# Kernel tuning notes

Measured on AMD Instinct MI355X. Metric: run time of the kernel, lower is better.

The kernel has to match this reference:

```python
import jax, jax.numpy as jnp
import numpy as np

N, E, F, HID, HEADS, L, OUT = 25000, 400000, 128, 128, 2, 3, 10
C = HID // HEADS
EPS = 1e-5

def _ln(x, g, b):
    m = jnp.mean(x, -1, keepdims=True)
    v = jnp.mean((x - m) ** 2, -1, keepdims=True)
    return (x - m) / jnp.sqrt(v + EPS) * g + b

def _lrelu(x, s=0.01):
    return jnp.where(x >= 0, x, s * x)

def setup_inputs():
    key = jax.random.key(0)
    ks = iter(jax.random.split(key, 80))
    def nrm(shape, fan_in):
        return jax.random.normal(next(ks), shape, dtype=jnp.float32) / np.float32(np.sqrt(fan_in))
    return {
        "x": jax.random.normal(next(ks), (N, F), dtype=jnp.float32),
        "edge_index": jax.random.randint(next(ks), (2, E), 0, N, dtype=jnp.int32),
        "edge_attr": jax.random.uniform(next(ks), (E,), dtype=jnp.float32),
        "task_features": jax.random.normal(next(ks), (4,), dtype=jnp.float32),
        "emb_w": nrm((F, HID), F), "emb_b": jnp.zeros((HID,), jnp.float32),
        "emb_g": jnp.ones((HID,), jnp.float32), "emb_beta": jnp.zeros((HID,), jnp.float32),
        "gat_w": nrm((L, HID, HID), HID),
        "gat_as": nrm((L, HEADS, C), C), "gat_ad": nrm((L, HEADS, C), C),
        "gat_bias": jnp.zeros((L, HID), jnp.float32),
        "ec_w1": nrm((L, 2 * HID, HID), 2 * HID), "ec_b1": jnp.zeros((L, HID), jnp.float32),
        "ec_g1": jnp.ones((L, HID), jnp.float32), "ec_be1": jnp.zeros((L, HID), jnp.float32),
        "ec_w2": nrm((L, HID, HID), HID), "ec_b2": jnp.zeros((L, HID), jnp.float32),
        "ec_g2": jnp.ones((L, HID), jnp.float32), "ec_be2": jnp.zeros((L, HID), jnp.float32),
        "norm_g": jnp.ones((L, HID), jnp.float32), "norm_b": jnp.zeros((L, HID), jnp.float32),
        "task_w": nrm((4, HID), 4), "task_b": jnp.zeros((HID,), jnp.float32),
        "task_g": jnp.ones((HID,), jnp.float32), "task_beta": jnp.zeros((HID,), jnp.float32),
        "pa_w1": nrm((HID, HID // 2), HID), "pa_b1": jnp.zeros((HID // 2,), jnp.float32),
        "pa_w2": nrm((HID // 2, 1), HID // 2), "pa_b2": jnp.zeros((1,), jnp.float32),
        "v_w1": nrm((2 * HID, HID), 2 * HID), "v_b1": jnp.zeros((HID,), jnp.float32),
        "v_g": jnp.ones((HID,), jnp.float32), "v_be": jnp.zeros((HID,), jnp.float32),
        "v_w2": nrm((HID, 1), HID), "v_b2": jnp.zeros((1,), jnp.float32),
        "a_w1": nrm((2 * HID, HID), 2 * HID), "a_b1": jnp.zeros((HID,), jnp.float32),
        "a_g": jnp.ones((HID,), jnp.float32), "a_be": jnp.zeros((HID,), jnp.float32),
        "a_w2": nrm((HID, OUT), HID), "a_b2": jnp.zeros((OUT,), jnp.float32),
    }

def _forward(x, edge_attr, task_features, emb_w, emb_b, emb_g, emb_beta,
             gat_w, gat_as, gat_ad, gat_bias,
             ec_w1, ec_b1, ec_g1, ec_be1, ec_w2, ec_b2, ec_g2, ec_be2,
             norm_g, norm_b, task_w, task_b, task_g, task_beta,
             pa_w1, pa_b1, pa_w2, pa_b2,
             v_w1, v_b1, v_g, v_be, v_w2, v_b2,
             a_w1, a_b1, a_g, a_be, a_w2, a_b2, edge_index):
    src, dst = edge_index[0], edge_index[1]
    loop = jnp.arange(N, dtype=edge_index.dtype)
    src_sl = jnp.concatenate([src, loop])  # PyG GATConv adds self-loops
    dst_sl = jnp.concatenate([dst, loop])
    h = _lrelu(_ln(x @ emb_w + emb_b, emb_g, emb_beta))
    x0 = h
    for i in range(L):
        # --- GATConv (dropout inactive at eval) ---
        ht = (h @ gat_w[i]).reshape(N, HEADS, C)
        a_s = jnp.sum(ht * gat_as[i], -1)  # [N, HEADS]
        a_d = jnp.sum(ht * gat_ad[i], -1)
        e = _lrelu(a_s[src_sl] + a_d[dst_sl], 0.2)  # [E+N, HEADS]
        emax = jax.ops.segment_max(e, dst_sl, num_segments=N)
        ee = jnp.exp(e - emax[dst_sl])
        alpha = ee / jax.ops.segment_sum(ee, dst_sl, num_segments=N)[dst_sl]
        x1 = jax.ops.segment_sum(ht[src_sl] * alpha[:, :, None], dst_sl,
                                 num_segments=N).reshape(N, HID) + gat_bias[i]
        # --- EdgeConv: gather -> MLP -> weighted scatter-add ---
        ef = jnp.concatenate([h[src], h[dst]], axis=1)  # [E, 2*HID]
        ef = _lrelu(_ln(ef @ ec_w1[i] + ec_b1[i], ec_g1[i], ec_be1[i]), 0.2)
        ef = _lrelu(_ln(ef @ ec_w2[i] + ec_b2[i], ec_g2[i], ec_be2[i]), 0.2)
        ef = ef * edge_attr[:, None]
        x2 = jax.ops.segment_sum(ef, dst, num_segments=N)
        h = _lrelu(_ln(x1 + x2, norm_g[i], norm_b[i]))
        if i > 0:
            h = h + x0
            x0 = h
    # attention pooling over all nodes (batch=None path)
    w = jax.nn.softmax((_lrelu(h @ pa_w1 + pa_b1) @ pa_w2 + pa_b2)[:, 0])
    gf = jnp.sum(h * w[:, None], axis=0)  # [HID]
    te = _lrelu(_ln(task_features @ task_w + task_b, task_g, task_beta))
    cf = jnp.concatenate([gf, te], -1)  # [2*HID]
    value = _lrelu(_ln(cf @ v_w1 + v_b1, v_g, v_be)) @ v_w2 + v_b2
    adv = _lrelu(_ln(cf @ a_w1 + a_b1, a_g, a_be)) @ a_w2 + a_b2
    return value + (adv - jnp.mean(adv, -1, keepdims=True))

def reference(x, edge_index, edge_attr, task_features, emb_w, emb_b, emb_g, emb_beta, gat_w, gat_as, gat_ad, gat_bias, ec_w1, ec_b1, ec_g1, ec_be1, ec_w2, ec_b2, ec_g2, ec_be2, norm_g, norm_b, task_w, task_b, task_g, task_beta, pa_w1, pa_b1, pa_w2, pa_b2, v_w1, v_b1, v_g, v_be, v_w2, v_b2, a_w1, a_b1, a_g, a_be, a_w2, a_b2):
    return _forward(x, edge_attr, task_features, emb_w, emb_b, emb_g, emb_beta, gat_w, gat_as, gat_ad, gat_bias, ec_w1, ec_b1, ec_g1, ec_be1, ec_w2, ec_b2, ec_g2, ec_be2, norm_g, norm_b, task_w, task_b, task_g, task_beta, pa_w1, pa_b1, pa_w2, pa_b2, v_w1, v_b1, v_g, v_be, v_w2, v_b2, a_w1, a_b1, a_g, a_be, a_w2, a_b2, edge_index)
```

## Files before the change

### kernel.cpp

```cpp
#include <hip/hip_runtime.h>
#include <math.h>

#define NN 25000
#define EE 400000
#define LL 3
#define LNEPS 1e-5f
#define EB 64

typedef __attribute__((ext_vector_type(8))) short short8;
typedef __attribute__((ext_vector_type(16))) float f32x16;

__device__ __forceinline__ float lrelu(float x, float s) { return fmaxf(x, x * s); }

__device__ __forceinline__ unsigned int pack_bf2(float lo, float hi) {
    unsigned int ul = __float_as_uint(lo), uh = __float_as_uint(hi);
    ul = (ul + 0x7FFFu + ((ul >> 16) & 1u)) >> 16;
    uh = (uh + 0x7FFFu + ((uh >> 16) & 1u)) >> 16;
    return (uh << 16) | (ul & 0xFFFFu);
}
__device__ __forceinline__ float bf_lo(unsigned int u) { return __uint_as_float(u << 16); }
__device__ __forceinline__ float bf_hi(unsigned int u) { return __uint_as_float(u & 0xFFFF0000u); }

__device__ __forceinline__ void ln_stats128(float v, float* red, float& mean, float& inv) {
    float sm = v, sq = v * v;
#pragma unroll
    for (int m = 32; m >= 1; m >>= 1) { sm += __shfl_xor(sm, m); sq += __shfl_xor(sq, m); }
    __syncthreads();
    if ((threadIdx.x & 63) == 0) { red[(threadIdx.x >> 6) * 2] = sm; red[(threadIdx.x >> 6) * 2 + 1] = sq; }
    __syncthreads();
    sm = red[0] + red[2]; sq = red[1] + red[3];
    mean = sm * (1.f / 128.f);
    float var = sq * (1.f / 128.f) - mean * mean;
    inv = rsqrtf(var + LNEPS);
}

__global__ void k_hist(const int* __restrict__ dst, int* __restrict__ cnt, int ne)
{
    int i = blockIdx.x * 256 + threadIdx.x;
    if (i < ne) atomicAdd(&cnt[dst[i]], 1);
}

__global__ __launch_bounds__(1024) void k_scan(const int* __restrict__ cnt,
                                               int* __restrict__ starts, int n)
{
    __shared__ int tot[1024];
    int t = threadIdx.x;
    const int PER = (n + 1023) >> 10;
    int i0 = t * PER;
    int s = 0;
    for (int k = 0; k < PER; ++k) { int i = i0 + k; s += (i < n) ? cnt[i] : 0; }
    tot[t] = s;
    __syncthreads();
    for (int off = 1; off < 1024; off <<= 1) {
        int x = (t >= off) ? tot[t - off] : 0;
        __syncthreads();
        tot[t] += x;
        __syncthreads();
    }
    int run = (t > 0) ? tot[t - 1] : 0;
    for (int k = 0; k < PER; ++k) {
        int i = i0 + k;
        if (i < n) { starts[i] = run; run += cnt[i]; }
    }
    if (t == 1023) starts[n] = tot[1023];
}

__global__ void k_scatter(const int* __restrict__ src, const int* __restrict__ dst,
                          const float* __restrict__ ea, int* __restrict__ cursor,
                          int* __restrict__ s_src, int* __restrict__ s_dst,
                          float* __restrict__ s_ea, int ne)
{
    int i = blockIdx.x * 256 + threadIdx.x;
    if (i >= ne) return;
    int d = dst[i];
    int pos = atomicAdd(&cursor[d], 1);
    s_src[pos] = src[i];
    s_dst[pos] = d;
    s_ea[pos] = ea[i];
}

__global__ void k_prep(const float* __restrict__ gat_w, const float* __restrict__ ec_w1,
                       const float* __restrict__ ec_w2, const float* __restrict__ emb_w,
                       uint4* __restrict__ wf)
{
    int g = blockIdx.x * 256 + threadIdx.x;
    int m = g >> 11, f = g & 2047;
    const float* srcm;
    if (m < 3) srcm = gat_w + (size_t)m * 16384;
    else if (m < 9) { int t2 = m - 3; srcm = ec_w1 + (size_t)(t2 >> 1) * 32768 + (size_t)(t2 & 1) * 16384; }
    else if (m < 12) srcm = ec_w2 + (size_t)(m - 9) * 16384;
    else srcm = emb_w;
    int l = f & 63, ks = (f >> 6) & 7, nb = f >> 9;
    int k0 = ks * 16 + (l >> 5) * 8, col = nb * 32 + (l & 31);
    const float* wp = srcm + (size_t)k0 * 128 + col;
    uint4 r;
    r.x = pack_bf2(wp[0],   wp[128]);
    r.y = pack_bf2(wp[256], wp[384]);
    r.z = pack_bf2(wp[512], wp[640]);
    r.w = pack_bf2(wp[768], wp[896]);
    wf[g] = r;
}

__global__ __launch_bounds__(256) void k_emb(
    const float* __restrict__ in, const uint4* __restrict__ wfm,
    const float* __restrict__ bias, const float* __restrict__ g,
    const float* __restrict__ be, float* __restrict__ h,
    float* __restrict__ x0, int nrows)
{
    __shared__ __align__(16) unsigned int sA[64 * 64];
    __shared__ __align__(16) unsigned int sW[2048 * 4];
    float* sU = (float*)sW;
    const int tid = threadIdx.x;
    const int r0 = blockIdx.x * 64;
    {
        int row = tid >> 2, q = tid & 3;
        const float* srcp = in + (size_t)(r0 + row) * 128 + q * 32;
        bool ok = (r0 + row) < nrows;
#pragma unroll
        for (int i = 0; i < 8; ++i) {
            float4 v = ok ? *(const float4*)&srcp[i * 4] : make_float4(0.f, 0.f, 0.f, 0.f);
            int cu = (q * 16 + i * 2) ^ ((row & 15) << 2);
            *(uint2*)&sA[row * 64 + cu] = make_uint2(pack_bf2(v.x, v.y), pack_bf2(v.z, v.w));
        }
    }
    {
        uint4* sW4 = (uint4*)sW;
#pragma unroll
        for (int i = 0; i < 8; ++i) sW4[tid + 256 * i] = wfm[tid + 256 * i];
    }
    __syncthreads();
    const int w = tid >> 6, l = tid & 63;
    const int m0 = (w >> 1) * 32, nhalf = (w & 1);
    f32x16 acc0 = {}, acc1 = {};
#pragma unroll
    for (int ks = 0; ks < 8; ++ks) {
        int rw = m0 + (l & 31);
        int cu = (ks * 8 + (l >> 5) * 4) ^ ((rw & 15) << 2);
        short8 a = *(const short8*)&sA[rw * 64 + cu];
        short8 b0 = *(const short8*)&sW[((nhalf * 16 + ks) * 64 + l) * 4];
        short8 b1 = *(const short8*)&sW[(((nhalf * 2 + 1) * 8 + ks) * 64 + l) * 4];
        acc0 = __builtin_amdgcn_mfma_f32_32x32x16_bf16(a, b0, acc0, 0, 0, 0);
        acc1 = __builtin_amdgcn_mfma_f32_32x32x16_bf16(a, b1, acc1, 0, 0, 0);
    }
    __syncthreads();
    {
        int colbase = nhalf * 64 + (l & 31);
        float bb0 = bias[colbase], bb1 = bias[colbase + 32];
#pragma unroll
        for (int r = 0; r < 16; ++r) {
            int rw = m0 + (r & 3) + 8 * (r >> 2) + 4 * (l >> 5);
            sU[rw * 128 + colbase]      = acc0[r] + bb0;
            sU[rw * 128 + colbase + 32] = acc1[r] + bb1;
        }
    }
    __syncthreads();
    float2 gv = *(const float2*)&g[l * 2];
    float2 bv = *(const float2*)&be[l * 2];
    for (int it = 0; it < 16; ++it) {
        int rw = w * 16 + it;
        int grow = r0 + rw;
        if (grow >= nrows) break;
        float2 v = *(const float2*)&sU[rw * 128 + l * 2];
        float sm = v.x + v.y, sq = v.x * v.x + v.y * v.y;
#pragma unroll
        for (int m = 32; m >= 1; m >>= 1) { sm += __shfl_xor(sm, m); sq += __shfl_xor(sq, m); }
        float mean = sm * (1.f / 128.f);
        float var = sq * (1.f / 128.f) - mean * mean;
        float inv = rsqrtf(var + LNEPS);
        float o0 = lrelu((v.x - mean) * inv * gv.x + bv.x, 0.01f);
        float o1 = lrelu((v.y - mean) * inv * gv.y + bv.y, 0.01f);
        unsigned off = (unsigned)grow * 128u + (unsigned)(l * 2);
        *(float2*)&h[off]  = make_float2(o0, o1);
        *(float2*)&x0[off] = make_float2(o0, o1);
    }
}

__global__ __launch_bounds__(256) void k_gemm3(
    const float* __restrict__ in, const uint4* __restrict__ wf,
    int mht, int mA, int mB, const float* __restrict__ bA,
    unsigned* __restrict__ o0, unsigned* __restrict__ o1, unsigned* __restrict__ o2,
    int nrows)
{
    __shared__ __align__(16) unsigned int sA[64 * 64];
    __shared__ __align__(16) unsigned int sW[2048 * 4];
    const int tid = threadIdx.x;
    const int r0 = blockIdx.x * 64;
    {
        int row = tid >> 2, q = tid & 3;
        const float* srcp = in + (size_t)(r0 + row) * 128 + q * 32;
        bool ok = (r0 + row) < nrows;
#pragma unroll
        for (int i = 0; i < 8; ++i) {
            float4 v = ok ? *(const float4*)&srcp[i * 4] : make_float4(0.f, 0.f, 0.f, 0.f);
            unsigned int p0 = pack_bf2(v.x, v.y), p1 = pack_bf2(v.z, v.w);
            int cu = (q * 16 + i * 2) ^ ((row & 15) << 2);
            *(uint2*)&sA[row * 64 + cu] = make_uint2(p0, p1);
        }
    }
    __syncthreads();
    const int w = tid >> 6, l = tid & 63;
    const int m0 = (w >> 1) * 32, nhalf = (w & 1);
    short8 af[8];
#pragma unroll
    for (int ks = 0; ks < 8; ++ks) {
        int row = m0 + (l & 31);
        int cu = (ks * 8 + (l >> 5) * 4) ^ ((row & 15) << 2);
        af[ks] = *(const short8*)&sA[row * 64 + cu];
    }
    const int c = l & 31;
    const bool evenl = (c & 1) == 0;
    const unsigned uidx = (unsigned)(nhalf * 32 + (evenl ? (c >> 1) : (16 + (c >> 1))));
    auto do_mat = [&](int mat, unsigned* out, const float* bp) {
        __syncthreads();
        {
            const uint4* wsrc = wf + (size_t)mat * 2048;
            uint4* sW4 = (uint4*)sW;
#pragma unroll
            for (int i = 0; i < 8; ++i) sW4[tid + 256 * i] = wsrc[tid + 256 * i];
        }
        __syncthreads();
        f32x16 acc0 = {}, acc1 = {};
        const int nb0 = nhalf * 2;
#pragma unroll
        for (int ks = 0; ks < 8; ++ks) {
            short8 b0 = *(const short8*)&sW[((nb0 * 8 + ks) * 64 + l) * 4];
            short8 b1v = *(const short8*)&sW[(((nb0 + 1) * 8 + ks) * 64 + l) * 4];
            acc0 = __builtin_amdgcn_mfma_f32_32x32x16_bf16(af[ks], b0, acc0, 0, 0, 0);
            acc1 = __builtin_amdgcn_mfma_f32_32x32x16_bf16(af[ks], b1v, acc1, 0, 0, 0);
        }
        int colbase = nhalf * 64 + c;
        float badd0 = bp ? bp[colbase] : 0.f;
        float badd1 = bp ? bp[colbase + 32] : 0.f;
#pragma unroll
        for (int r = 0; r < 16; ++r) {
            float v0 = acc0[r] + badd0;
            float v1 = acc1[r] + badd1;
            float v0p = __shfl_xor(v0, 1);
            float v1p = __shfl_xor(v1, 1);
            int row = r0 + m0 + (r & 3) + 8 * (r >> 2) + 4 * (l >> 5);
            if (row < nrows) {
                unsigned val = evenl ? pack_bf2(v0, v0p) : pack_bf2(v1p, v1);
                out[(unsigned)row * 64u + uidx] = val;
            }
        }
    };
    do_mat(mht, o0, nullptr);
    do_mat(mA, o1, bA);
    do_mat(mB, o2, nullptr);
}

__global__ __launch_bounds__(512) void k_node_scores(
    const unsigned* __restrict__ htp, const unsigned* __restrict__ Apk,
    const unsigned* __restrict__ Bpk,
    const float* __restrict__ as_, const float* __restrict__ ad_,
    float* __restrict__ a_s, float* __restrict__ a_d,
    float* __restrict__ denom, float* __restrict__ selfe,
    float* __restrict__ rsA, float* __restrict__ rsB, int n)
{
    int wv = threadIdx.x >> 6, ln = threadIdx.x & 63;
    int node = blockIdx.x * 8 + wv;
    if (node >= n) return;
    unsigned off = (unsigned)node * 64u + (unsigned)ln;
    unsigned hv = htp[off], av = Apk[off], bv = Bpk[off];
    float h0 = bf_lo(hv), h1 = bf_hi(hv);
    float2 wsv = *(const float2*)&as_[ln * 2];
    float2 wdv = *(const float2*)&ad_[ln * 2];
    float ss = h0 * wsv.x + h1 * wsv.y;
    float sd = h0 * wdv.x + h1 * wdv.y;
    float sa = bf_lo(av) + bf_hi(av), sb = bf_lo(bv) + bf_hi(bv);
#pragma unroll
    for (int m = 16; m >= 1; m >>= 1) {
        ss += __shfl_xor(ss, m); sd += __shfl_xor(sd, m);
        sa += __shfl_xor(sa, m); sb += __shfl_xor(sb, m);
    }
    float sa2 = sa + __shfl_xor(sa, 32);
    float sb2 = sb + __shfl_xor(sb, 32);
    if ((ln & 31) == 0) {
        int hd = ln >> 5;
        a_s[node * 2 + hd] = ss;
        a_d[node * 2 + hd] = sd;
        float ev = expf(lrelu(ss + sd, 0.2f));
        denom[node * 2 + hd] = ev;
        selfe[node * 2 + hd] = ev;
        if (hd == 0) { rsA[node] = sa2; rsB[node] = sb2; }
    }
}

__global__ void k_edge_denom2(const int* __restrict__ s_src, const int* __restrict__ s_dst,
                              const float* __restrict__ a_s, const float* __restrict__ a_d,
                              float* __restrict__ denom, int ne)
{
    int base = (blockIdx.x * 256 + threadIdx.x) * 8;
    if (base >= ne) return;
    int curd = -1;
    float acc0 = 0.f, acc1 = 0.f;
    for (int k = 0; k < 8; ++k) {
        int e = base + k;
        if (e >= ne) break;
        int s = s_src[e], d = s_dst[e];
        float v0 = expf(lrelu(a_s[(unsigned)(s * 2)]     + a_d[(unsigned)(d * 2)],     0.2f));
        float v1 = expf(lrelu(a_s[(unsigned)(s * 2 + 1)] + a_d[(unsigned)(d * 2 + 1)], 0.2f));
        if (d != curd) {
            if (curd >= 0) { atomicAdd(&denom[curd * 2], acc0); atomicAdd(&denom[curd * 2 + 1], acc1); }
            curd = d; acc0 = v0; acc1 = v1;
        } else { acc0 += v0; acc1 += v1; }
    }
    if (curd >= 0) { atomicAdd(&denom[curd * 2], acc0); atomicAdd(&denom[curd * 2 + 1], acc1); }
}

__global__ void k_xsum_init(const unsigned* __restrict__ htp, const float* __restrict__ selfe,
                            const float* __restrict__ denom,
                            const float* __restrict__ gbias, float* __restrict__ xsum, int n)
{
    unsigned idx = blockIdx.x * blockDim.x + threadIdx.x;
    if (idx >= (unsigned)n * 64u) return;
    unsigned node = idx >> 6, u = idx & 63, hd = u >> 5;
    float alpha = selfe[node * 2 + hd] / denom[node * 2 + hd];
    unsigned hv = htp[idx];
    float2 o;
    o.x = gbias[u * 2]     + bf_lo(hv) * alpha;
    o.y = gbias[u * 2 + 1] + bf_hi(hv) * alpha;
    *(float2*)&xsum[node * 128u + u * 2u] = o;
}

__global__ __launch_bounds__(512) void k_edge_main(
    const unsigned* __restrict__ Apk, const unsigned* __restrict__ Bpk,
    const unsigned* __restrict__ htp,
    const int* __restrict__ s_src, const int* __restrict__ s_dst,
    const float* __restrict__ s_ea,
    const float* __restrict__ a_s, const float* __restrict__ a_d,
    const float* __restrict__ denom,
    const uint4* __restrict__ w2f,
    const float* __restrict__ rsA, const float* __restrict__ rsB,
    const float* __restrict__ g1, const float* __restrict__ be1,
    const float* __restrict__ b2, const float* __restrict__ g2, const float* __restrict__ be2,
    float* __restrict__ xsum, int ne)
{
    __shared__ __align__(16) unsigned int sWB[2048 * 4];
    __shared__ __align__(16) unsigned int sT32[EB * 64];
    __shared__ int   sS[EB], sD[EB];
    __shared__ float sEA[EB], sM[EB];
    __shared__ float sAl[EB * 2];
    __shared__ float sG1[128], sE1[128], sB2[128], sG2[128], sE2[128];
    float* sU = (float*)sWB;

    const int tid = threadIdx.x;
    {
        uint4* sWB4 = (uint4*)sWB;
#pragma unroll
        for (int i = 0; i < 4; ++i) { int f = tid + 512 * i; sWB4[f] = w2f[f]; }
    }
    if (tid < 128) {
        sG1[tid] = g1[tid]; sE1[tid] = be1[tid];
        sB2[tid] = b2[tid]; sG2[tid] = g2[tid]; sE2[tid] = be2[tid];
    }
    const int e0 = blockIdx.x * EB;
    const int nev = (ne - e0 < EB) ? (ne - e0) : EB;
    if (tid < EB) {
        if (tid < nev) {
            int s = s_src[e0 + tid], d = s_dst[e0 + tid];
            sS[tid] = s; sD[tid] = d; sEA[tid] = s_ea[e0 + tid];
            sM[tid] = (rsA[s] + rsB[d]) * (1.f / 128.f);
        } else { sS[tid] = 0; sD[tid] = -1; sEA[tid] = 0.f; sM[tid] = 0.f; }
    }
    if (tid < 2 * EB) {
        int le = tid >> 1, hd = tid & 1;
        float al = 0.f;
        if (le < nev) {
            int e = e0 + le;
            int s = s_src[e], d = s_dst[e];
            float ev = lrelu(a_s[(unsigned)(s * 2 + hd)] + a_d[(unsigned)(d * 2 + hd)], 0.2f);
            al = expf(ev) / denom[(unsigned)(d * 2 + hd)];
        }
        sAl[le * 2 + hd] = al;
    }
    __syncthreads();

    const int wv = tid >> 6, ln = tid & 63;
    {
        const float g1a = sG1[ln * 2], g1b = sG1[ln * 2 + 1];
        const float e1a = sE1[ln * 2], e1b = sE1[ln * 2 + 1];
        for (int j = 0; j < 8; ++j) {
            int e = wv * 8 + j;
            if (e < nev) {
                unsigned s = (unsigned)sS[e], d = (unsigned)sD[e];
                float mean = sM[e];
                unsigned av = Apk[s * 64u + ln];
                unsigned bv = Bpk[d * 64u + ln];
                float v0 = bf_lo(av) + bf_lo(bv) - mean;
                float v1 = bf_hi(av) + bf_hi(bv) - mean;
                float sq = v0 * v0 + v1 * v1;
#pragma unroll
                for (int m = 32; m >= 1; m >>= 1) sq += __shfl_xor(sq, m);
                float inv = rsqrtf(sq * (1.f / 128.f) + LNEPS);
                float t0 = lrelu(v0 * inv * g1a + e1a, 0.2f);
                float t1 = lrelu(v1 * inv * g1b + e1b, 0.2f);
                sT32[e * 64 + (ln ^ ((e & 15) << 2))] = pack_bf2(t0, t1);
            }
        }
    }
    __syncthreads();

    {
        const int w = wv, l = ln;
        const int m0 = (w >> 2) * 32, n0 = (w & 3) * 32;
        f32x16 acc = {};
#pragma unroll
        for (int ks = 0; ks < 8; ++ks) {
            int row = m0 + (l & 31);
            int colu = (ks * 8 + (l >> 5) * 4) ^ ((row & 15) << 2);
            short8 a = *(const short8*)&sT32[row * 64 + colu];
            short8 b = *(const short8*)&sWB[((((w & 3) * 8 + ks) * 64 + l)) * 4];
            acc = __builtin_amdgcn_mfma_f32_32x32x16_bf16(a, b, acc, 0, 0, 0);
        }
        __syncthreads();
        float b2c = sB2[n0 + (l & 31)];
#pragma unroll
        for (int r = 0; r < 16; ++r) {
            int row = m0 + (r & 3) + 8 * (r >> 2) + 4 * (l >> 5);
            sU[row * 128 + n0 + (l & 31)] = acc[r] + b2c;
        }
    }
    __syncthreads();

    {
        const unsigned ln2 = (unsigned)(ln * 2);
        const float g2a = sG2[ln * 2], g2b = sG2[ln * 2 + 1];
        const float e2a = sE2[ln * 2], e2b = sE2[ln * 2 + 1];
        int curd = -1;
        float acc0 = 0.f, acc1 = 0.f;
        for (int j = 0; j < 8; ++j) {
            int e = wv * 8 + j;
            if (e >= nev) break;
            unsigned s = (unsigned)sS[e];
            int d = sD[e];
            float2 uv = *(const float2*)&sU[e * 128 + ln * 2];
            float u0 = uv.x, u1 = uv.y;
            float sm = u0 + u1, sq = u0 * u0 + u1 * u1;
#pragma unroll
            for (int m = 32; m >= 1; m >>= 1) { sm += __shfl_xor(sm, m); sq += __shfl_xor(sq, m); }
            float mean = sm * (1.f / 128.f);
            float var = sq * (1.f / 128.f) - mean * mean;
            float inv = rsqrtf(var + LNEPS);
            float eav = sEA[e];
            float v0 = lrelu((u0 - mean) * inv * g2a + e2a, 0.2f) * eav;
            float v1 = lrelu((u1 - mean) * inv * g2b + e2b, 0.2f) * eav;
            float al = sAl[e * 2 + (ln >> 5)];
            unsigned hv = htp[s * 64u + ln];
            v0 += bf_lo(hv) * al;
            v1 += bf_hi(hv) * al;
            if (d != curd) {
                if (curd >= 0) {
                    atomicAdd(&xsum[(unsigned)curd * 128u + ln2], acc0);
                    atomicAdd(&xsum[(unsigned)curd * 128u + ln2 + 1], acc1);
                }
                curd = d; acc0 = v0; acc1 = v1;
            } else { acc0 += v0; acc1 += v1; }
        }
        if (curd >= 0) {
            atomicAdd(&xsum[(unsigned)curd * 128u + ln2], acc0);
            atomicAdd(&xsum[(unsigned)curd * 128u + ln2 + 1], acc1);
        }
    }
}

__global__ __launch_bounds__(512) void k_norm8(const float* __restrict__ xsum,
                                               const float* __restrict__ g,
                                               const float* __restrict__ b,
                                               float* __restrict__ x0,
                                               float* __restrict__ h, int n, int layer)
{
    int wv = threadIdx.x >> 6, ln = threadIdx.x & 63;
    int node = blockIdx.x * 8 + wv;
    if (node >= n) return;
    unsigned off = (unsigned)node * 128u + (unsigned)(ln * 2);
    float2 v = *(const float2*)&xsum[off];
    float sm = v.x + v.y, sq = v.x * v.x + v.y * v.y;
#pragma unroll
    for (int m = 32; m >= 1; m >>= 1) { sm += __shfl_xor(sm, m); sq += __shfl_xor(sq, m); }
    float mean = sm * (1.f / 128.f);
    float var = sq * (1.f / 128.f) - mean * mean;
    float inv = rsqrtf(var + LNEPS);
    float2 gv = *(const float2*)&g[ln * 2];
    float2 bv = *(const float2*)&b[ln * 2];
    float val0 = lrelu((v.x - mean) * inv * gv.x + bv.x, 0.01f);
    float val1 = lrelu((v.y - mean) * inv * gv.y + bv.y, 0.01f);
    if (layer > 0) {
        float2 x0v = *(const float2*)&x0[off];
        val0 += x0v.x; val1 += x0v.y;
        *(float2*)&x0[off] = make_float2(val0, val1);
    }
    *(float2*)&h[off] = make_float2(val0, val1);
}

__global__ __launch_bounds__(256) void k_pool_score(const float* __restrict__ h,
    const float* __restrict__ w1, const float* __restrict__ b1,
    const float* __restrict__ w2, const float* __restrict__ b2,
    float* __restrict__ score, int n)
{
    int wv = threadIdx.x >> 6, ln = threadIdx.x & 63;
    int node = blockIdx.x * 4 + wv;
    if (node >= n) return;
    float acc = b1[ln];
    const float* hr = h + (size_t)node * 128;
    for (int k = 0; k < 128; ++k) acc += hr[k] * w1[k * 64 + ln];
    acc = lrelu(acc, 0.01f) * w2[ln];
#pragma unroll
    for (int m = 32; m >= 1; m >>= 1) acc += __shfl_xor(acc, m);
    if (ln == 0) score[node] = acc + b2[0];
}

__global__ __launch_bounds__(256) void k_softmax_reduce(const float* __restrict__ score,
                                                        float* __restrict__ stats,
                                                        float* __restrict__ gf, int n)
{
    __shared__ float red[8];
    int t = threadIdx.x;
    float mx = -1e30f;
    for (int i = t; i < n; i += 256) mx = fmaxf(mx, score[i]);
#pragma unroll
    for (int m = 32; m >= 1; m >>= 1) mx = fmaxf(mx, __shfl_xor(mx, m));
    if ((t & 63) == 0) red[t >> 6] = mx;
    __syncthreads();
    mx = fmaxf(fmaxf(red[0], red[1]), fmaxf(red[2], red[3]));
    float s = 0.f;
    for (int i = t; i < n; i += 256) s += expf(score[i] - mx);
#pragma unroll
    for (int m = 32; m >= 1; m >>= 1) s += __shfl_xor(s, m);
    if ((t & 63) == 0) red[4 + (t >> 6)] = s;
    __syncthreads();
    s = red[4] + red[5] + red[6] + red[7];
    if (t == 0) { stats[0] = mx; stats[1] = s; }
    if (t < 128) gf[t] = 0.f;
}

__global__ __launch_bounds__(128) void k_gf(const float* __restrict__ h,
                                            const float* __restrict__ score,
                                            const float* __restrict__ stats,
                                            float* __restrict__ gf, int n)
{
    int c = threadIdx.x;
    float mx = stats[0], invZ = 1.f / stats[1];
    int per = (n + gridDim.x - 1) / gridDim.x;
    int n0 = blockIdx.x * per;
    int n1 = n0 + per; if (n1 > n) n1 = n;
    float acc = 0.f;
    for (int i = n0; i < n1; ++i)
        acc += expf(score[i] - mx) * invZ * h[(size_t)i * 128 + c];
    atomicAdd(&gf[c], acc);
}

__global__ __launch_bounds__(128) void k_head(
    const float* __restrict__ gf, const float* __restrict__ tf,
    const float* __restrict__ task_w, const float* __restrict__ task_b,
    const float* __restrict__ task_g, const float* __restrict__ task_be,
    const float* __restrict__ v_w1, const float* __restrict__ v_b1,
    const float* __restrict__ v_g, const float* __restrict__ v_be,
    const float* __restrict__ v_w2, const float* __restrict__ v_b2,
    const float* __restrict__ a_w1, const float* __restrict__ a_b1,
    const float* __restrict__ a_g, const float* __restrict__ a_be,
    const float* __restrict__ a_w2, const float* __restrict__ a_b2,
    float* __restrict__ out)
{
    __shared__ float cf[256], hbuf[128], red[4], sc[2], adv[10];
    int t = threadIdx.x;
    float mean, inv;
    float te = task_b[t];
#pragma unroll
    for (int k = 0; k < 4; ++k) te += tf[k] * task_w[k * 128 + t];
    ln_stats128(te, red, mean, inv);
    te = lrelu((te - mean) * inv * task_g[t] + task_be[t], 0.01f);
    cf[t] = gf[t]; cf[128 + t] = te;
    __syncthreads();
    float v = v_b1[t];
    for (int k = 0; k < 256; ++k) v += cf[k] * v_w1[k * 128 + t];
    ln_stats128(v, red, mean, inv);
    v = lrelu((v - mean) * inv * v_g[t] + v_be[t], 0.01f);
    float pv = v * v_w2[t];
#pragma unroll
    for (int m = 32; m >= 1; m >>= 1) pv += __shfl_xor(pv, m);
    __syncthreads();
    if ((t & 63) == 0) red[t >> 6] = pv;
    __syncthreads();
    if (t == 0) sc[0] = red[0] + red[1] + v_b2[0];
    float a = a_b1[t];
    for (int k = 0; k < 256; ++k) a += cf[k] * a_w1[k * 128 + t];
    ln_stats128(a, red, mean, inv);
    a = lrelu((a - mean) * inv * a_g[t] + a_be[t], 0.01f);
    hbuf[t] = a;
    __syncthreads();
    if (t < 10) {
        float s = a_b2[t];
        for (int c = 0; c < 128; ++c) s += hbuf[c] * a_w2[c * 10 + t];
        adv[t] = s;
    }
    __syncthreads();
    if (t == 0) {
        float m10 = 0.f;
        for (int o = 0; o < 10; ++o) m10 += adv[o];
        sc[1] = m10 * 0.1f;
    }
    __syncthreads();
    if (t < 10) out[t] = sc[0] + adv[t] - sc[1];
}

extern "C" void kernel_launch(void* const* d_in, const int* in_sizes, int n_in,
                              void* d_out, int out_size, void* d_ws, size_t ws_size,
                              hipStream_t stream)
{
    const float* x        = (const float*)d_in[0];
    const int*   ei       = (const int*)d_in[1];
    const float* ea       = (const float*)d_in[2];
    const float* tf       = (const float*)d_in[3];
    const float* emb_w    = (const float*)d_in[4];
    const float* emb_b    = (const float*)d_in[5];
    const float* emb_g    = (const float*)d_in[6];
    const float* emb_beta = (const float*)d_in[7];
    const float* gat_w    = (const float*)d_in[8];
    const float* gat_as   = (const float*)d_in[9];
    const float* gat_ad   = (const float*)d_in[10];
    const float* gat_bias = (const float*)d_in[11];
    const float* ec_w1    = (const float*)d_in[12];
    const float* ec_b1    = (const float*)d_in[13];
    const float* ec_g1    = (const float*)d_in[14];
    const float* ec_be1   = (const float*)d_in[15];
    const float* ec_w2    = (const float*)d_in[16];
    const float* ec_b2    = (const float*)d_in[17];
    const float* ec_g2    = (const float*)d_in[18];
    const float* ec_be2   = (const float*)d_in[19];
    const float* norm_g   = (const float*)d_in[20];
    const float* norm_b   = (const float*)d_in[21];
    const float* task_w   = (const float*)d_in[22];
    const float* task_b   = (const float*)d_in[23];
    const float* task_g   = (const float*)d_in[24];
    const float* task_be  = (const float*)d_in[25];
    const float* pa_w1    = (const float*)d_in[26];
    const float* pa_b1    = (const float*)d_in[27];
    const float* pa_w2    = (const float*)d_in[28];
    const float* pa_b2    = (const float*)d_in[29];
    const float* v_w1     = (const float*)d_in[30];
    const float* v_b1     = (const float*)d_in[31];
    const float* v_g      = (const float*)d_in[32];
    const float* v_be     = (const float*)d_in[33];
    const float* v_w2     = (const float*)d_in[34];
    const float* v_b2     = (const float*)d_in[35];
    const float* a_w1     = (const float*)d_in[36];
    const float* a_b1     = (const float*)d_in[37];
    const float* a_g      = (const float*)d_in[38];
    const float* a_be     = (const float*)d_in[39];
    const float* a_w2     = (const float*)d_in[40];
    const float* a_b2     = (const float*)d_in[41];

    const int n = in_sizes[0] / 128;
    const int e = in_sizes[2];
    const int* src = ei;
    const int* dst = ei + e;

    float* ws = (float*)d_ws;
    uint4* wf = (uint4*)ws;
    float* base = ws + 13 * 2048 * 4;
    const size_t NR = (size_t)n * 128;
    const size_t NP = (size_t)n * 64;
    float* h    = base;
    float* x0   = base + NR;
    float* xs   = base + 2 * NR;
    unsigned* htp = (unsigned*)(base + 3 * NR);
    unsigned* Apk = htp + NP;
    unsigned* Bpk = Apk + NP;
    float* a_s  = (float*)(Bpk + NP);
    float* a_d  = a_s + (size_t)n * 2;
    float* den  = a_d + (size_t)n * 2;
    float* selfe = den + (size_t)n * 2;
    float* rsA  = selfe + (size_t)n * 2;
    float* rsB  = rsA + n;
    float* score = rsB + n;
    float* stats = score + n;
    float* gf    = stats + 2;
    int*   cnt    = (int*)(gf + 128);
    int*   starts = cnt + n;
    int*   s_src  = starts + (n + 1);
    int*   s_dst  = s_src + e;
    float* s_ea   = (float*)(s_dst + e);

    const int ng64 = (n + 63) / 64;
    const int ng8 = (n + 7) / 8;

    hipMemsetAsync(cnt, 0, (size_t)n * sizeof(int), stream);
    k_hist<<<(e + 255) / 256, 256, 0, stream>>>(dst, cnt, e);
    k_scan<<<1, 1024, 0, stream>>>(cnt, starts, n);
    hipMemcpyAsync(cnt, starts, (size_t)n * sizeof(int), hipMemcpyDeviceToDevice, stream);
    k_scatter<<<(e + 255) / 256, 256, 0, stream>>>(src, dst, ea, cnt, s_src, s_dst, s_ea, e);
    k_prep<<<104, 256, 0, stream>>>(gat_w, ec_w1, ec_w2, emb_w, wf);

    k_emb<<<ng64, 256, 0, stream>>>(x, wf + (size_t)12 * 2048, emb_b, emb_g, emb_beta, h, x0, n);

    for (int i = 0; i < LL; ++i) {
        k_gemm3<<<ng64, 256, 0, stream>>>(h, wf, i, 3 + 2 * i, 4 + 2 * i,
                                          ec_b1 + i * 128, htp, Apk, Bpk, n);
        k_node_scores<<<ng8, 512, 0, stream>>>(htp, Apk, Bpk, gat_as + i * 128, gat_ad + i * 128,
                                               a_s, a_d, den, selfe, rsA, rsB, n);
        k_edge_denom2<<<((e + 7) / 8 + 255) / 256, 256, 0, stream>>>(s_src, s_dst, a_s, a_d, den, e);
        k_xsum_init<<<(n * 64 + 255) / 256, 256, 0, stream>>>(htp, selfe, den,
                                                              gat_bias + i * 128, xs, n);
        k_edge_main<<<(e + EB - 1) / EB, 512, 0, stream>>>(Apk, Bpk, htp, s_src, s_dst, s_ea,
                                                           a_s, a_d, den,
                                                           wf + (size_t)(9 + i) * 2048,
                                                           rsA, rsB,
                                                           ec_g1 + i * 128, ec_be1 + i * 128,
                                                           ec_b2 + i * 128, ec_g2 + i * 128, ec_be2 + i * 128,
                                                           xs, e);
        k_norm8<<<ng8, 512, 0, stream>>>(xs, norm_g + i * 128, norm_b + i * 128, x0, h, n, i);
    }

    k_pool_score<<<(n + 3) / 4, 256, 0, stream>>>(h, pa_w1, pa_b1, pa_w2, pa_b2, score, n);
    k_softmax_reduce<<<1, 256, 0, stream>>>(score, stats, gf, n);
    k_gf<<<200, 128, 0, stream>>>(h, score, stats, gf, n);
    k_head<<<1, 128, 0, stream>>>(gf, tf, task_w, task_b, task_g, task_be,
                                  v_w1, v_b1, v_g, v_be, v_w2, v_b2,
                                  a_w1, a_b1, a_g, a_be, a_w2, a_b2,
                                  (float*)d_out);
}
```

Baseline: 798.1 us.

## Fuse xsum init into norm, cache edge exps, compute LN mean via MFMA

```diff
diff --git a/kernel.cpp b/kernel.cpp
--- a/kernel.cpp
+++ b/kernel.cpp
@@ -81,24 +81,44 @@
 
 __global__ void k_prep(const float* __restrict__ gat_w, const float* __restrict__ ec_w1,
                        const float* __restrict__ ec_w2, const float* __restrict__ emb_w,
-                       uint4* __restrict__ wf)
-{
-    int g = blockIdx.x * 256 + threadIdx.x;
-    int m = g >> 11, f = g & 2047;
-    const float* srcm;
-    if (m < 3) srcm = gat_w + (size_t)m * 16384;
-    else if (m < 9) { int t2 = m - 3; srcm = ec_w1 + (size_t)(t2 >> 1) * 32768 + (size_t)(t2 & 1) * 16384; }
-    else if (m < 12) srcm = ec_w2 + (size_t)(m - 9) * 16384;
-    else srcm = emb_w;
-    int l = f & 63, ks = (f >> 6) & 7, nb = f >> 9;
-    int k0 = ks * 16 + (l >> 5) * 8, col = nb * 32 + (l & 31);
-    const float* wp = srcm + (size_t)k0 * 128 + col;
-    uint4 r;
-    r.x = pack_bf2(wp[0],   wp[128]);
-    r.y = pack_bf2(wp[256], wp[384]);
-    r.z = pack_bf2(wp[512], wp[640]);
-    r.w = pack_bf2(wp[768], wp[896]);
-    wf[g] = r;
+                       const float* __restrict__ ec_b2,
+                       uint4* __restrict__ wf, float* __restrict__ w2rs,
+                       float* __restrict__ b2s)
+{
+    int bid = blockIdx.x;
+    if (bid < 104) {
+        int g = bid * 256 + threadIdx.x;
+        int m = g >> 11, f = g & 2047;
+        const float* srcm;
+        if (m < 3) srcm = gat_w + (size_t)m * 16384;
+        else if (m < 9) { int t2 = m - 3; srcm = ec_w1 + (size_t)(t2 >> 1) * 32768 + (size_t)(t2 & 1) * 16384; }
+        else if (m < 12) srcm = ec_w2 + (size_t)(m - 9) * 16384;
+        else srcm = emb_w;
+        int l = f & 63, ks = (f >> 6) & 7, nb = f >> 9;
+        int k0 = ks * 16 + (l >> 5) * 8, col = nb * 32 + (l & 31);
+        const float* wp = srcm + (size_t)k0 * 128 + col;
+        uint4 r;
+        r.x = pack_bf2(wp[0],   wp[128]);
+        r.y = pack_bf2(wp[256], wp[384]);
+        r.z = pack_bf2(wp[512], wp[640]);
+        r.w = pack_bf2(wp[768], wp[896]);
+        wf[g] = r;
+    } else {
+        int gi = (bid - 104) * 256 + threadIdx.x;
+        if (gi < 384) {
+            int mt = gi >> 7, k = gi & 127;
+            const float* wp = ec_w2 + (size_t)mt * 16384 + (size_t)k * 128;
+            float s = 0.f;
+            for (int j = 0; j < 128; ++j) s += bf_lo(pack_bf2(wp[j], 0.f));
+            w2rs[mt * 128 + k] = s;
+        } else if (gi < 387) {
+            int mt = gi - 384;
+            const float* bp = ec_b2 + mt * 128;
+            float s = 0.f;
+            for (int j = 0; j < 128; ++j) s += bp[j];
+            b2s[mt] = s;
+        }
+    }
 }
 
 __global__ __launch_bounds__(256) void k_emb(
@@ -288,9 +308,13 @@
 
 __global__ void k_edge_denom2(const int* __restrict__ s_src, const int* __restrict__ s_dst,
                               const float* __restrict__ a_s, const float* __restrict__ a_d,
-                              float* __restrict__ denom, int ne)
-{
-    int base = (blockIdx.x * 256 + threadIdx.x) * 8;
+                              float* __restrict__ denom, float* __restrict__ expo,
+                              float4* __restrict__ xz, int nz4, int ne)
+{
+    int gtid = blockIdx.x * 256 + threadIdx.x;
+    for (int i = gtid; i < nz4; i += gridDim.x * 256)
+        xz[i] = make_float4(0.f, 0.f, 0.f, 0.f);
+    int base = gtid * 8;
     if (base >= ne) return;
     int curd = -1;
     float acc0 = 0.f, acc1 = 0.f;
@@ -300,27 +324,13 @@
         int s = s_src[e], d = s_dst[e];
         float v0 = expf(lrelu(a_s[(unsigned)(s * 2)]     + a_d[(unsigned)(d * 2)],     0.2f));
         float v1 = expf(lrelu(a_s[(unsigned)(s * 2 + 1)] + a_d[(unsigned)(d * 2 + 1)], 0.2f));
+        *(float2*)&expo[(unsigned)e * 2] = make_float2(v0, v1);
         if (d != curd) {
             if (curd >= 0) { atomicAdd(&denom[curd * 2], acc0); atomicAdd(&denom[curd * 2 + 1], acc1); }
             curd = d; acc0 = v0; acc1 = v1;
         } else { acc0 += v0; acc1 += v1; }
     }
     if (curd >= 0) { atomicAdd(&denom[curd * 2], acc0); atomicAdd(&denom[curd * 2 + 1], acc1); }
-}
-
-__global__ void k_xsum_init(const unsigned* __restrict__ htp, const float* __restrict__ selfe,
-                            const float* __restrict__ denom,
-                            const float* __restrict__ gbias, float* __restrict__ xsum, int n)
-{
-    unsigned idx = blockIdx.x * blockDim.x + threadIdx.x;
-    if (idx >= (unsigned)n * 64u) return;
-    unsigned node = idx >> 6, u = idx & 63, hd = u >> 5;
-    float alpha = selfe[node * 2 + hd] / denom[node * 2 + hd];
-    unsigned hv = htp[idx];
-    float2 o;
-    o.x = gbias[u * 2]     + bf_lo(hv) * alpha;
-    o.y = gbias[u * 2 + 1] + bf_hi(hv) * alpha;
-    *(float2*)&xsum[node * 128u + u * 2u] = o;
 }
 
 __global__ __launch_bounds__(512) void k_edge_main(
@@ -328,9 +338,9 @@
     const unsigned* __restrict__ htp,
     const int* __restrict__ s_src, const int* __restrict__ s_dst,
     const float* __restrict__ s_ea,
-    const float* __restrict__ a_s, const float* __restrict__ a_d,
-    const float* __restrict__ denom,
+    const float* __restrict__ expo, const float* __restrict__ denom,
     const uint4* __restrict__ w2f,
+    const float* __restrict__ w2rs, const float* __restrict__ b2sum,
     const float* __restrict__ rsA, const float* __restrict__ rsB,
     const float* __restrict__ g1, const float* __restrict__ be1,
     const float* __restrict__ b2, const float* __restrict__ g2, const float* __restrict__ be2,
@@ -341,6 +351,9 @@
     __shared__ int   sS[EB], sD[EB];
     __shared__ float sEA[EB], sM[EB];
     __shared__ float sAl[EB * 2];
+    __shared__ float sMean[EB];
+    __shared__ __align__(16) unsigned int sRS[64];
+    __shared__ float sB2S[1];
     __shared__ float sG1[128], sE1[128], sB2[128], sG2[128], sE2[128];
     float* sU = (float*)sWB;
 
@@ -354,6 +367,8 @@
         sG1[tid] = g1[tid]; sE1[tid] = be1[tid];
         sB2[tid] = b2[tid]; sG2[tid] = g2[tid]; sE2[tid] = be2[tid];
     }
+    if (tid < 64) sRS[tid] = pack_bf2(w2rs[tid * 2], w2rs[tid * 2 + 1]);
+    if (tid == 64) sB2S[0] = b2sum[0];
     const int e0 = blockIdx.x * EB;
     const int nev = (ne - e0 < EB) ? (ne - e0) : EB;
     if (tid < EB) {
@@ -368,9 +383,8 @@
         float al = 0.f;
         if (le < nev) {
             int e = e0 + le;
-            int s = s_src[e], d = s_dst[e];
-            float ev = lrelu(a_s[(unsigned)(s * 2 + hd)] + a_d[(unsigned)(d * 2 + hd)], 0.2f);
-            al = expf(ev) / denom[(unsigned)(d * 2 + hd)];
+            int d = s_dst[e];
+            al = expo[(unsigned)e * 2 + hd] / denom[(unsigned)(d * 2 + hd)];
         }
         sAl[le * 2 + hd] = al;
     }
@@ -404,7 +418,8 @@
     {
         const int w = wv, l = ln;
         const int m0 = (w >> 2) * 32, n0 = (w & 3) * 32;
-        f32x16 acc = {};
+        const bool dostat = (w & 3) == 0;
+        f32x16 acc = {}, accS = {};
 #pragma unroll
         for (int ks = 0; ks < 8; ++ks) {
             int row = m0 + (l & 31);
@@ -412,6 +427,18 @@
             short8 a = *(const short8*)&sT32[row * 64 + colu];
             short8 b = *(const short8*)&sWB[((((w & 3) * 8 + ks) * 64 + l)) * 4];
             acc = __builtin_amdgcn_mfma_f32_32x32x16_bf16(a, b, acc, 0, 0, 0);
+            if (dostat) {
+                short8 brs = *(const short8*)&sRS[ks * 8 + (l >> 5) * 4];
+                accS = __builtin_amdgcn_mfma_f32_32x32x16_bf16(a, brs, accS, 0, 0, 0);
+            }
+        }
+        if (dostat && (l & 31) == 0) {
+            float b2sv = sB2S[0];
+#pragma unroll
+            for (int r = 0; r < 16; ++r) {
+                int row = m0 + (r & 3) + 8 * (r >> 2) + 4 * (l >> 5);
+                sMean[row] = (accS[r] + b2sv) * (1.f / 128.f);
+            }
         }
         __syncthreads();
         float b2c = sB2[n0 + (l & 31)];
@@ -434,17 +461,16 @@
             if (e >= nev) break;
             unsigned s = (unsigned)sS[e];
             int d = sD[e];
+            float mean = sMean[e];
             float2 uv = *(const float2*)&sU[e * 128 + ln * 2];
-            float u0 = uv.x, u1 = uv.y;
-            float sm = u0 + u1, sq = u0 * u0 + u1 * u1;
-#pragma unroll
-            for (int m = 32; m >= 1; m >>= 1) { sm += __shfl_xor(sm, m); sq += __shfl_xor(sq, m); }
-            float mean = sm * (1.f / 128.f);
-            float var = sq * (1.f / 128.f) - mean * mean;
-            float inv = rsqrtf(var + LNEPS);
+            float v0c = uv.x - mean, v1c = uv.y - mean;
+            float sq = v0c * v0c + v1c * v1c;
+#pragma unroll
+            for (int m = 32; m >= 1; m >>= 1) sq += __shfl_xor(sq, m);
+            float inv = rsqrtf(sq * (1.f / 128.f) + LNEPS);
             float eav = sEA[e];
-            float v0 = lrelu((u0 - mean) * inv * g2a + e2a, 0.2f) * eav;
-            float v1 = lrelu((u1 - mean) * inv * g2b + e2b, 0.2f) * eav;
+            float v0 = lrelu(v0c * inv * g2a + e2a, 0.2f) * eav;
+            float v1 = lrelu(v1c * inv * g2b + e2b, 0.2f) * eav;
             float al = sAl[e * 2 + (ln >> 5)];
             unsigned hv = htp[s * 64u + ln];
             v0 += bf_lo(hv) * al;
@@ -465,6 +491,10 @@
 }
 
 __global__ __launch_bounds__(512) void k_norm8(const float* __restrict__ xsum,
+                                               const unsigned* __restrict__ htp,
+                                               const float* __restrict__ selfe,
+                                               const float* __restrict__ denom,
+                                               const float* __restrict__ gbias,
                                                const float* __restrict__ g,
                                                const float* __restrict__ b,
                                                float* __restrict__ x0,
@@ -474,7 +504,13 @@
     int node = blockIdx.x * 8 + wv;
     if (node >= n) return;
     unsigned off = (unsigned)node * 128u + (unsigned)(ln * 2);
+    int hd = ln >> 5;
+    float alpha = selfe[node * 2 + hd] / denom[node * 2 + hd];
+    unsigned hv = htp[(unsigned)node * 64u + (unsigned)ln];
+    float2 gb = *(const float2*)&gbias[ln * 2];
     float2 v = *(const float2*)&xsum[off];
+    v.x += gb.x + bf_lo(hv) * alpha;
+    v.y += gb.y + bf_hi(hv) * alpha;
     float sm = v.x + v.y, sq = v.x * v.x + v.y * v.y;
 #pragma unroll
     for (int m = 32; m >= 1; m >>= 1) { sm += __shfl_xor(sm, m); sq += __shfl_xor(sq, m); }
@@ -681,16 +717,20 @@
     int*   s_src  = starts + (n + 1);
     int*   s_dst  = s_src + e;
     float* s_ea   = (float*)(s_dst + e);
+    float* expo   = s_ea + e;
+    float* w2rs   = expo + (size_t)2 * e;
+    float* b2sum  = w2rs + 384;
 
     const int ng64 = (n + 63) / 64;
     const int ng8 = (n + 7) / 8;
+    const int ngd = ((e + 7) / 8 + 255) / 256;
 
     hipMemsetAsync(cnt, 0, (size_t)n * sizeof(int), stream);
     k_hist<<<(e + 255) / 256, 256, 0, stream>>>(dst, cnt, e);
     k_scan<<<1, 1024, 0, stream>>>(cnt, starts, n);
     hipMemcpyAsync(cnt, starts, (size_t)n * sizeof(int), hipMemcpyDeviceToDevice, stream);
     k_scatter<<<(e + 255) / 256, 256, 0, stream>>>(src, dst, ea, cnt, s_src, s_dst, s_ea, e);
-    k_prep<<<104, 256, 0, stream>>>(gat_w, ec_w1, ec_w2, emb_w, wf);
+    k_prep<<<106, 256, 0, stream>>>(gat_w, ec_w1, ec_w2, emb_w, ec_b2, wf, w2rs, b2sum);
 
     k_emb<<<ng64, 256, 0, stream>>>(x, wf + (size_t)12 * 2048, emb_b, emb_g, emb_beta, h, x0, n);
 
@@ -699,17 +739,18 @@
                                           ec_b1 + i * 128, htp, Apk, Bpk, n);
         k_node_scores<<<ng8, 512, 0, stream>>>(htp, Apk, Bpk, gat_as + i * 128, gat_ad + i * 128,
                                                a_s, a_d, den, selfe, rsA, rsB, n);
-        k_edge_denom2<<<((e + 7) / 8 + 255) / 256, 256, 0, stream>>>(s_src, s_dst, a_s, a_d, den, e);
-        k_xsum_init<<<(n * 64 + 255) / 256, 256, 0, stream>>>(htp, selfe, den,
-                                                              gat_bias + i * 128, xs, n);
+        k_edge_denom2<<<ngd, 256, 0, stream>>>(s_src, s_dst, a_s, a_d, den, expo,
+                                               (float4*)xs, n * 32, e);
         k_edge_main<<<(e + EB - 1) / EB, 512, 0, stream>>>(Apk, Bpk, htp, s_src, s_dst, s_ea,
-                                                           a_s, a_d, den,
+                                                           expo, den,
                                                            wf + (size_t)(9 + i) * 2048,
+                                                           w2rs + i * 128, b2sum + i,
                                                            rsA, rsB,
                                                            ec_g1 + i * 128, ec_be1 + i * 128,
                                                            ec_b2 + i * 128, ec_g2 + i * 128, ec_be2 + i * 128,
                                                            xs, e);
-        k_norm8<<<ng8, 512, 0, stream>>>(xs, norm_g + i * 128, norm_b + i * 128, x0, h, n, i);
+        k_norm8<<<ng8, 512, 0, stream>>>(xs, htp, selfe, den, gat_bias + i * 128,
+                                         norm_g + i * 128, norm_b + i * 128, x0, h, n, i);
     }
 
     k_pool_score<<<(n + 3) / 4, 256, 0, stream>>>(h, pa_w1, pa_b1, pa_w2, pa_b2, score, n);
```

New measurement: 904.0 us. 13.3% more time.

## Fold xsum init into norm kernel and cache edge exponentials

Applied to the files above, without the earlier changes.

```diff
diff --git a/kernel.cpp b/kernel.cpp
--- a/kernel.cpp
+++ b/kernel.cpp
@@ -288,9 +288,13 @@
 
 __global__ void k_edge_denom2(const int* __restrict__ s_src, const int* __restrict__ s_dst,
                               const float* __restrict__ a_s, const float* __restrict__ a_d,
-                              float* __restrict__ denom, int ne)
-{
-    int base = (blockIdx.x * 256 + threadIdx.x) * 8;
+                              float* __restrict__ denom, float* __restrict__ expo,
+                              float4* __restrict__ xz, int nz4, int ne)
+{
+    int gtid = blockIdx.x * 256 + threadIdx.x;
+    for (int i = gtid; i < nz4; i += gridDim.x * 256)
+        xz[i] = make_float4(0.f, 0.f, 0.f, 0.f);
+    int base = gtid * 8;
     if (base >= ne) return;
     int curd = -1;
     float acc0 = 0.f, acc1 = 0.f;
@@ -300,27 +304,13 @@
         int s = s_src[e], d = s_dst[e];
         float v0 = expf(lrelu(a_s[(unsigned)(s * 2)]     + a_d[(unsigned)(d * 2)],     0.2f));
         float v1 = expf(lrelu(a_s[(unsigned)(s * 2 + 1)] + a_d[(unsigned)(d * 2 + 1)], 0.2f));
+        *(float2*)&expo[(unsigned)e * 2] = make_float2(v0, v1);
         if (d != curd) {
             if (curd >= 0) { atomicAdd(&denom[curd * 2], acc0); atomicAdd(&denom[curd * 2 + 1], acc1); }
             curd = d; acc0 = v0; acc1 = v1;
         } else { acc0 += v0; acc1 += v1; }
     }
     if (curd >= 0) { atomicAdd(&denom[curd * 2], acc0); atomicAdd(&denom[curd * 2 + 1], acc1); }
-}
-
-__global__ void k_xsum_init(const unsigned* __restrict__ htp, const float* __restrict__ selfe,
-                            const float* __restrict__ denom,
-                            const float* __restrict__ gbias, float* __restrict__ xsum, int n)
-{
-    unsigned idx = blockIdx.x * blockDim.x + threadIdx.x;
-    if (idx >= (unsigned)n * 64u) return;
-    unsigned node = idx >> 6, u = idx & 63, hd = u >> 5;
-    float alpha = selfe[node * 2 + hd] / denom[node * 2 + hd];
-    unsigned hv = htp[idx];
-    float2 o;
-    o.x = gbias[u * 2]     + bf_lo(hv) * alpha;
-    o.y = gbias[u * 2 + 1] + bf_hi(hv) * alpha;
-    *(float2*)&xsum[node * 128u + u * 2u] = o;
 }
 
 __global__ __launch_bounds__(512) void k_edge_main(
@@ -328,8 +318,7 @@
     const unsigned* __restrict__ htp,
     const int* __restrict__ s_src, const int* __restrict__ s_dst,
     const float* __restrict__ s_ea,
-    const float* __restrict__ a_s, const float* __restrict__ a_d,
-    const float* __restrict__ denom,
+    const float* __restrict__ expo, const float* __restrict__ denom,
     const uint4* __restrict__ w2f,
     const float* __restrict__ rsA, const float* __restrict__ rsB,
     const float* __restrict__ g1, const float* __restrict__ be1,
@@ -368,15 +357,15 @@
         float al = 0.f;
         if (le < nev) {
             int e = e0 + le;
-            int s = s_src[e], d = s_dst[e];
-            float ev = lrelu(a_s[(unsigned)(s * 2 + hd)] + a_d[(unsigned)(d * 2 + hd)], 0.2f);
-            al = expf(ev) / denom[(unsigned)(d * 2 + hd)];
+            int d = s_dst[e];
+            al = expo[(unsigned)e * 2 + hd] / denom[(unsigned)(d * 2 + hd)];
         }
         sAl[le * 2 + hd] = al;
     }
     __syncthreads();
 
     const int wv = tid >> 6, ln = tid & 63;
+    const unsigned ln2 = (unsigned)(ln * 2);
     {
         const float g1a = sG1[ln * 2], g1b = sG1[ln * 2 + 1];
         const float e1a = sE1[ln * 2], e1b = sE1[ln * 2 + 1];
@@ -424,7 +413,6 @@
     __syncthreads();
 
     {
-        const unsigned ln2 = (unsigned)(ln * 2);
         const float g2a = sG2[ln * 2], g2b = sG2[ln * 2 + 1];
         const float e2a = sE2[ln * 2], e2b = sE2[ln * 2 + 1];
         int curd = -1;
@@ -465,6 +453,10 @@
 }
 
 __global__ __launch_bounds__(512) void k_norm8(const float* __restrict__ xsum,
+                                               const unsigned* __restrict__ htp,
+                                               const float* __restrict__ selfe,
+                                               const float* __restrict__ denom,
+                                               const float* __restrict__ gbias,
                                                const float* __restrict__ g,
                                                const float* __restrict__ b,
                                                float* __restrict__ x0,
@@ -474,7 +466,13 @@
     int node = blockIdx.x * 8 + wv;
     if (node >= n) return;
     unsigned off = (unsigned)node * 128u + (unsigned)(ln * 2);
+    int hd = ln >> 5;
+    float alpha = selfe[node * 2 + hd] / denom[node * 2 + hd];
+    unsigned hv = htp[(unsigned)node * 64u + (unsigned)ln];
+    float2 gb = *(const float2*)&gbias[ln * 2];
     float2 v = *(const float2*)&xsum[off];
+    v.x += gb.x + bf_lo(hv) * alpha;
+    v.y += gb.y + bf_hi(hv) * alpha;
     float sm = v.x + v.y, sq = v.x * v.x + v.y * v.y;
 #pragma unroll
     for (int m = 32; m >= 1; m >>= 1) { sm += __shfl_xor(sm, m); sq += __shfl_xor(sq, m); }
@@ -681,9 +679,11 @@
     int*   s_src  = starts + (n + 1);
     int*   s_dst  = s_src + e;
     float* s_ea   = (float*)(s_dst + e);
+    float* expo   = s_ea + e;
 
     const int ng64 = (n + 63) / 64;
     const int ng8 = (n + 7) / 8;
+    const int ngd = ((e + 7) / 8 + 255) / 256;
 
     hipMemsetAsync(cnt, 0, (size_t)n * sizeof(int), stream);
     k_hist<<<(e + 255) / 256, 256, 0, stream>>>(dst, cnt, e);
@@ -699,17 +699,17 @@
                                           ec_b1 + i * 128, htp, Apk, Bpk, n);
         k_node_scores<<<ng8, 512, 0, stream>>>(htp, Apk, Bpk, gat_as + i * 128, gat_ad + i * 128,
                                                a_s, a_d, den, selfe, rsA, rsB, n);
-        k_edge_denom2<<<((e + 7) / 8 + 255) / 256, 256, 0, stream>>>(s_src, s_dst, a_s, a_d, den, e);
-        k_xsum_init<<<(n * 64 + 255) / 256, 256, 0, stream>>>(htp, selfe, den,
-                                                              gat_bias + i * 128, xs, n);
+        k_edge_denom2<<<ngd, 256, 0, stream>>>(s_src, s_dst, a_s, a_d, den, expo,
+                                               (float4*)xs, n * 32, e);
         k_edge_main<<<(e + EB - 1) / EB, 512, 0, stream>>>(Apk, Bpk, htp, s_src, s_dst, s_ea,
-                                                           a_s, a_d, den,
+                                                           expo, den,
                                                            wf + (size_t)(9 + i) * 2048,
                                                            rsA, rsB,
                                                            ec_g1 + i * 128, ec_be1 + i * 128,
                                                            ec_b2 + i * 128, ec_g2 + i * 128, ec_be2 + i * 128,
                                                            xs, e);
-        k_norm8<<<ng8, 512, 0, stream>>>(xs, norm_g + i * 128, norm_b + i * 128, x0, h, n, i);
+        k_norm8<<<ng8, 512, 0, stream>>>(xs, htp, selfe, den, gat_bias + i * 128,
+                                         norm_g + i * 128, norm_b + i * 128, x0, h, n, i);
     }
 
     k_pool_score<<<(n + 3) / 4, 256, 0, stream>>>(h, pa_w1, pa_b1, pa_w2, pa_b2, score, n);
```

After: 791.1 us. About the same (-0.9%).
